# Optimization experiments

Hardware: AMD Instinct MI355X
Metric: run time of the kernel (lower is better)

## Reference

```python
import jax, jax.numpy as jnp
import numpy as np

SIGMA = 0.4  # hp.guided_attention_sigma


def setup_inputs() -> dict:
    key = jax.random.key(0)
    k1, k2, k3 = jax.random.split(key, 3)
    B, T, S = 32, 2048, 512  # batch, trg(mel) len, src(text) len
    source_len = jax.random.randint(k1, (B,), 1, S + 1)
    target_len = jax.random.randint(k2, (B,), 1, T + 1)
    predict_attns = jax.random.uniform(k3, (B, T, S), dtype=jnp.float32)
    return {"source_len": source_len, "target_len": target_len,
            "predict_attns": predict_attns}


def reference(source_len, target_len, predict_attns):
    B, T, S = predict_attns.shape
    # grid_x indexes the output (trg) axis, grid_y the input (src) axis
    x = jnp.arange(T, dtype=jnp.float32)[None, :, None]  # [1,T,1]
    y = jnp.arange(S, dtype=jnp.float32)[None, None, :]  # [1,1,S]
    ilen = source_len.astype(jnp.float32)[:, None, None]  # [B,1,1]
    olen = target_len.astype(jnp.float32)[:, None, None]  # [B,1,1]
    # guided attention weight, zero-padded outside each sample's (olen, ilen) box
    w = 1.0 - jnp.exp(-((y / ilen - x / olen) ** 2) / (2.0 * SIGMA ** 2))
    valid = (x < olen) & (y < ilen)  # [B,T,S] non-pad mask
    w = jnp.where(valid, w, 0.0)
    # masked_select(...).mean(): sum over valid positions / count of valid positions
    num = jnp.sum(w * predict_attns)
    den = jnp.sum(valid).astype(jnp.float32)
    return num / den
```

## Files before the change

kernel.cpp:

```cpp
#include <hip/hip_runtime.h>
#include <hip/hip_bf16.h>


#define GA_T 2048
#define GA_S 512
#define GA_INV2S2 (1.0f / (2.0f * 0.4f * 0.4f))

#define BLOCK 256
#define NBLK 2048
#define GA_B 32

__global__ __launch_bounds__(BLOCK) void ga_partial_kernel(
    const int* __restrict__ slen, const int* __restrict__ tlen,
    const float* __restrict__ p, float* __restrict__ partial) {
  __shared__ unsigned pref[GA_B + 1];
  __shared__ unsigned Wsh[GA_B];
  __shared__ int ilsh[GA_B];
  __shared__ float inv_il_sh[GA_B], inv_ol_sh[GA_B];
  __shared__ unsigned szsh[GA_B];

  if (threadIdx.x < GA_B) {
    const int b = threadIdx.x;
    const int il = slen[b];
    const int ol = tlen[b];
    const unsigned W = (unsigned)((il + 3) >> 2);
    Wsh[b] = W;
    ilsh[b] = il;
    inv_il_sh[b] = 1.0f / (float)il;
    inv_ol_sh[b] = 1.0f / (float)ol;
    szsh[b] = W * (unsigned)ol;
  }
  __syncthreads();
  if (threadIdx.x == 0) {
    unsigned run = 0;
#pragma unroll
    for (int b = 0; b < GA_B; ++b) { pref[b] = run; run += szsh[b]; }
    pref[GA_B] = run;
  }
  __syncthreads();

  const unsigned S_tot = pref[GA_B];
  const unsigned chunk = (S_tot + NBLK - 1) / NBLK;
  const unsigned start = blockIdx.x * chunk;
  const unsigned end = (start + chunk < S_tot) ? (start + chunk) : S_tot;

  float acc = 0.0f;

  for (unsigned q = start + threadIdx.x; q < end; q += BLOCK) {
    int b = 0;
#pragma unroll
    for (int step = 16; step > 0; step >>= 1)
      if (pref[b + step] <= q) b += step;

    const unsigned qr = q - pref[b];
    const unsigned W = Wsh[b];
    const unsigned t = qr / W;
    const unsigned sv = qr - t * W;
    const int s0 = (int)(sv << 2);
    const int il = ilsh[b];
    const float inv_il = inv_il_sh[b];
    const float xo = (float)t * inv_ol_sh[b];

    const float4 pv = *reinterpret_cast<const float4*>(
        p + ((size_t)(b * GA_T + (int)t) * GA_S + s0));

    const float d0 = (float)(s0 + 0) * inv_il - xo;
    const float d1 = (float)(s0 + 1) * inv_il - xo;
    const float d2 = (float)(s0 + 2) * inv_il - xo;
    const float d3 = (float)(s0 + 3) * inv_il - xo;
    const float e0 = __expf(-(d0 * d0) * GA_INV2S2);
    const float e1 = __expf(-(d1 * d1) * GA_INV2S2);
    const float e2 = __expf(-(d2 * d2) * GA_INV2S2);
    const float e3 = __expf(-(d3 * d3) * GA_INV2S2);
    const float p0 = pv.x;
    const float p1 = (s0 + 1 < il) ? pv.y : 0.0f;
    const float p2 = (s0 + 2 < il) ? pv.z : 0.0f;
    const float p3 = (s0 + 3 < il) ? pv.w : 0.0f;
    acc += p0 - p0 * e0;
    acc += p1 - p1 * e1;
    acc += p2 - p2 * e2;
    acc += p3 - p3 * e3;
  }

  for (int off = 32; off > 0; off >>= 1)
    acc += __shfl_down(acc, off, 64);

  __shared__ float wsum[BLOCK / 64];
  const int lane = threadIdx.x & 63;
  const int wid = threadIdx.x >> 6;
  if (lane == 0) wsum[wid] = acc;
  __syncthreads();

  if (threadIdx.x == 0)
    partial[blockIdx.x] = (wsum[0] + wsum[1]) + (wsum[2] + wsum[3]);
}

__global__ __launch_bounds__(64) void ga_final_kernel(
    const int* __restrict__ slen, const int* __restrict__ tlen,
    const float* __restrict__ partial, int B, float* __restrict__ out) {
  const int lane = threadIdx.x;

  double s = 0.0;
#pragma unroll
  for (int k = 0; k < NBLK / (64 * 4); ++k) {
    const float4 f =
        *reinterpret_cast<const float4*>(partial + (k * 64 + lane) * 4);
    s += ((double)f.x + (double)f.y) + ((double)f.z + (double)f.w);
  }

  double den = 0.0;
  if (lane < B) den = (double)slen[lane] * (double)tlen[lane];

#pragma unroll
  for (int off = 32; off > 0; off >>= 1) {
    s += __shfl_down(s, off, 64);
    den += __shfl_down(den, off, 64);
  }

  if (lane == 0) out[0] = (float)(s / den);
}

extern "C" void kernel_launch(void* const* d_in, const int* in_sizes, int n_in,
                              void* d_out, int out_size, void* d_ws, size_t ws_size,
                              hipStream_t stream) {
  const int* slen = (const int*)d_in[0];
  const int* tlen = (const int*)d_in[1];
  const float* p = (const float*)d_in[2];
  float* out = (float*)d_out;
  float* partial = (float*)d_ws;

  const int B = in_sizes[0];

  ga_partial_kernel<<<NBLK, BLOCK, 0, stream>>>(slen, tlen, p, partial);
  ga_final_kernel<<<1, 64, 0, stream>>>(slen, tlen, partial, B, out);
}
```

Baseline: 14.40 us.

## Batch four float4 loads per thread, use wave-scan prefix and nontemporal loads

The main loop is restructured so each thread issues four independent nontemporal vector loads before doing the exp arithmetic, which raises memory-level parallelism. Out-of-range slots are clamped to a valid address and zeroed with float masks rather than branches. The serial single-thread prefix sum over batch sizes is replaced by a wavefront shuffle scan, removing one barrier. The final kernel now loads all partials up front before the double-precision sums. Clamped slots add redundant loads and extra register pressure.

```diff
diff --git a/kernel.cpp b/kernel.cpp
--- a/kernel.cpp
+++ b/kernel.cpp
@@ -10,6 +10,8 @@
 #define NBLK 2048
 #define GA_B 32
 
+typedef float f32x4 __attribute__((ext_vector_type(4)));
+
 __global__ __launch_bounds__(BLOCK) void ga_partial_kernel(
     const int* __restrict__ slen, const int* __restrict__ tlen,
     const float* __restrict__ p, float* __restrict__ partial) {
@@ -17,69 +19,89 @@
   __shared__ unsigned Wsh[GA_B];
   __shared__ int ilsh[GA_B];
   __shared__ float inv_il_sh[GA_B], inv_ol_sh[GA_B];
-  __shared__ unsigned szsh[GA_B];
 
-  if (threadIdx.x < GA_B) {
-    const int b = threadIdx.x;
-    const int il = slen[b];
-    const int ol = tlen[b];
-    const unsigned W = (unsigned)((il + 3) >> 2);
-    Wsh[b] = W;
-    ilsh[b] = il;
-    inv_il_sh[b] = 1.0f / (float)il;
-    inv_ol_sh[b] = 1.0f / (float)ol;
-    szsh[b] = W * (unsigned)ol;
-  }
-  __syncthreads();
-  if (threadIdx.x == 0) {
-    unsigned run = 0;
+  const int tid = threadIdx.x;
+
+  if (tid < 64) {
+    unsigned sz = 0;
+    if (tid < GA_B) {
+      const int il = slen[tid];
+      const int ol = tlen[tid];
+      const unsigned W = (unsigned)((il + 3) >> 2);
+      Wsh[tid] = W;
+      ilsh[tid] = il;
+      inv_il_sh[tid] = 1.0f / (float)il;
+      inv_ol_sh[tid] = 1.0f / (float)ol;
+      sz = W * (unsigned)ol;
+    }
+    unsigned v = sz;
 #pragma unroll
-    for (int b = 0; b < GA_B; ++b) { pref[b] = run; run += szsh[b]; }
-    pref[GA_B] = run;
+    for (int d = 1; d < 32; d <<= 1) {
+      unsigned u = __shfl_up(v, d, 64);
+      v += (tid >= d) ? u : 0u;
+    }
+    if (tid < GA_B) pref[tid + 1] = v;
+    if (tid == 0) pref[0] = 0;
   }
   __syncthreads();
 
   const unsigned S_tot = pref[GA_B];
   const unsigned chunk = (S_tot + NBLK - 1) / NBLK;
-  const unsigned start = blockIdx.x * chunk;
+  const unsigned start = (unsigned)blockIdx.x * chunk;
   const unsigned end = (start + chunk < S_tot) ? (start + chunk) : S_tot;
+  const unsigned ITERS = (chunk + BLOCK - 1) / BLOCK;
 
   float acc = 0.0f;
 
-  for (unsigned q = start + threadIdx.x; q < end; q += BLOCK) {
-    int b = 0;
+  for (unsigned it0 = 0; it0 < ITERS; it0 += 4) {
+    f32x4 pv[4];
+    float xo[4], invil[4], ok[4], m1[4], m2[4], m3[4];
+    int s0v[4];
 #pragma unroll
-    for (int step = 16; step > 0; step >>= 1)
-      if (pref[b + step] <= q) b += step;
-
-    const unsigned qr = q - pref[b];
-    const unsigned W = Wsh[b];
-    const unsigned t = qr / W;
-    const unsigned sv = qr - t * W;
-    const int s0 = (int)(sv << 2);
-    const int il = ilsh[b];
-    const float inv_il = inv_il_sh[b];
-    const float xo = (float)t * inv_ol_sh[b];
-
-    const float4 pv = *reinterpret_cast<const float4*>(
-        p + ((size_t)(b * GA_T + (int)t) * GA_S + s0));
-
-    const float d0 = (float)(s0 + 0) * inv_il - xo;
-    const float d1 = (float)(s0 + 1) * inv_il - xo;
-    const float d2 = (float)(s0 + 2) * inv_il - xo;
-    const float d3 = (float)(s0 + 3) * inv_il - xo;
-    const float e0 = __expf(-(d0 * d0) * GA_INV2S2);
-    const float e1 = __expf(-(d1 * d1) * GA_INV2S2);
-    const float e2 = __expf(-(d2 * d2) * GA_INV2S2);
-    const float e3 = __expf(-(d3 * d3) * GA_INV2S2);
-    const float p0 = pv.x;
-    const float p1 = (s0 + 1 < il) ? pv.y : 0.0f;
-    const float p2 = (s0 + 2 < il) ? pv.z : 0.0f;
-    const float p3 = (s0 + 3 < il) ? pv.w : 0.0f;
-    acc += p0 - p0 * e0;
-    acc += p1 - p1 * e1;
-    acc += p2 - p2 * e2;
-    acc += p3 - p3 * e3;
+    for (int j = 0; j < 4; ++j) {
+      const unsigned it = it0 + (unsigned)j;
+      const unsigned q = start + it * BLOCK + (unsigned)tid;
+      const bool valid = (it < ITERS) && (q < end);
+      ok[j] = valid ? 1.0f : 0.0f;
+      const unsigned qc = valid ? q : (S_tot - 1);
+      int b = 0;
+#pragma unroll
+      for (int step = 16; step > 0; step >>= 1)
+        if (pref[b + step] <= qc) b += step;
+      const unsigned qr = qc - pref[b];
+      const unsigned W = Wsh[b];
+      const unsigned t = qr / W;
+      const unsigned sv = qr - t * W;
+      const int s0 = (int)(sv << 2);
+      const int il = ilsh[b];
+      s0v[j] = s0;
+      invil[j] = inv_il_sh[b];
+      xo[j] = (float)t * inv_ol_sh[b];
+      m1[j] = (s0 + 1 < il) ? 1.0f : 0.0f;
+      m2[j] = (s0 + 2 < il) ? 1.0f : 0.0f;
+      m3[j] = (s0 + 3 < il) ? 1.0f : 0.0f;
+      pv[j] = __builtin_nontemporal_load(reinterpret_cast<const f32x4*>(
+          p + ((size_t)(b * GA_T + (int)t) * GA_S + s0)));
+    }
+#pragma unroll
+    for (int j = 0; j < 4; ++j) {
+      const float d0 = (float)(s0v[j] + 0) * invil[j] - xo[j];
+      const float d1 = (float)(s0v[j] + 1) * invil[j] - xo[j];
+      const float d2 = (float)(s0v[j] + 2) * invil[j] - xo[j];
+      const float d3 = (float)(s0v[j] + 3) * invil[j] - xo[j];
+      const float e0 = __expf(-(d0 * d0) * GA_INV2S2);
+      const float e1 = __expf(-(d1 * d1) * GA_INV2S2);
+      const float e2 = __expf(-(d2 * d2) * GA_INV2S2);
+      const float e3 = __expf(-(d3 * d3) * GA_INV2S2);
+      const float p0 = ok[j] * pv[j][0];
+      const float p1 = ok[j] * m1[j] * pv[j][1];
+      const float p2 = ok[j] * m2[j] * pv[j][2];
+      const float p3 = ok[j] * m3[j] * pv[j][3];
+      acc += p0 - p0 * e0;
+      acc += p1 - p1 * e1;
+      acc += p2 - p2 * e2;
+      acc += p3 - p3 * e3;
+    }
   }
 
   for (int off = 32; off > 0; off >>= 1)
@@ -100,13 +122,16 @@
     const float* __restrict__ partial, int B, float* __restrict__ out) {
   const int lane = threadIdx.x;
 
+  f32x4 f[NBLK / (64 * 4)];
+#pragma unroll
+  for (int k = 0; k < NBLK / (64 * 4); ++k)
+    f[k] = *reinterpret_cast<const f32x4*>(partial + (k * 64 + lane) * 4);
+
   double s = 0.0;
 #pragma unroll
-  for (int k = 0; k < NBLK / (64 * 4); ++k) {
-    const float4 f =
-        *reinterpret_cast<const float4*>(partial + (k * 64 + lane) * 4);
-    s += ((double)f.x + (double)f.y) + ((double)f.z + (double)f.w);
-  }
+  for (int k = 0; k < NBLK / (64 * 4); ++k)
+    s += ((double)f[k][0] + (double)f[k][1]) +
+         ((double)f[k][2] + (double)f[k][3]);
 
   double den = 0.0;
   if (lane < B) den = (double)slen[lane] * (double)tlen[lane];
```

Measured after the change: 13.64 us. 5.3% less time.
